# Performance work log

Hardware: AMD Instinct MI355X
Metric: run time of the kernel (lower is better)

## Reference

```python
import jax, jax.numpy as jnp
import numpy as np

T, B, N = 512, 256, 128


def setup_inputs() -> dict:
    key = jax.random.key(0)
    k1, k2, k3, k4, k5, k6 = jax.random.split(key, 6)
    emit = jax.random.normal(k1, (T, B, N), dtype=jnp.float32)
    target = jax.random.randint(k2, (T, B), 0, N)
    # prefix-true mask from random lengths in [1, T]
    lengths = jax.random.randint(k3, (B,), 1, T + 1)
    mask = jnp.arange(T)[:, None] < lengths[None, :]
    std = (1.0 / N) ** 0.5
    trans = jax.random.normal(k4, (N, N), dtype=jnp.float32) * std
    strans = jax.random.normal(k5, (N,), dtype=jnp.float32) * std
    etrans = jax.random.normal(k6, (N,), dtype=jnp.float32) * std
    return {"emit": emit, "target": target, "mask": mask,
            "trans": trans, "strans": strans, "etrans": etrans}


def _logZ(emit, mask, trans, strans, etrans):
    alpha0 = strans + emit[0]  # (B, N)

    def step(alpha, xs):
        e_t, m_t = xs  # (B, N), (B,)
        # scores[b, j] = logsumexp_i(alpha[b, i] + trans[i, j] + e_t[b, j])
        scores = jax.scipy.special.logsumexp(
            alpha[:, :, None] + trans[None, :, :] + e_t[:, None, :], axis=1)
        alpha = jnp.where(m_t[:, None], scores, alpha)
        return alpha, None

    alpha, _ = jax.lax.scan(step, alpha0, (emit[1:], mask[1:]))
    return jax.scipy.special.logsumexp(alpha + etrans, axis=1).sum()


def _score(emit, target, mask, trans, strans, etrans):
    Tn, Bn, _ = emit.shape
    # emission scores of gold tags: (T, B)
    sc = jnp.take_along_axis(emit, target[:, :, None], axis=2)[..., 0]
    # transition scores between consecutive gold tags
    sc = sc.at[1:].add(trans[target[:-1], target[1:]])
    score = jnp.sum(jnp.where(mask, sc, jnp.float32(0.0)))
    ends = mask.astype(jnp.int32).sum(axis=0) - 1  # (B,)
    score = score + strans[target[0]].sum()
    score = score + etrans[target[ends, jnp.arange(Bn)]].sum()
    return score


def reference(emit, target, mask, trans, strans, etrans):
    Bn = emit.shape[1]
    logZ = _logZ(emit, mask, trans, strans, etrans)
    score = _score(emit, target, mask, trans, strans, etrans)
    return (logZ - score) / Bn
```

## Files before the change

### kernel.cpp

```cpp
#include <hip/hip_runtime.h>

#define TT 512
#define BB 256
#define NN 128
#define MW 16
#define NWG (BB / MW)
#define STH 144

#define LENS_OFF 256
#define AF_OFF 2048
#define CF_OFF (AF_OFF + BB * NN * 4)
#define BU_OFF (CF_OFF + 1024)
#define CB_OFF (BU_OFF + BB * NN * 4)
#define XQ_OFF (CB_OFF + 1024)
#define XQ_SZ ((size_t)TT * BB * NN * 2)

typedef __attribute__((ext_vector_type(8))) short short8_t;
typedef __attribute__((ext_vector_type(4))) float f32x4;

__device__ __forceinline__ unsigned short f2bf(float f) {
  unsigned u = __float_as_uint(f);
  return (unsigned short)((u + 0x7FFF + ((u >> 16) & 1)) >> 16);
}
__device__ __forceinline__ float bf2f(unsigned short h) {
  return __uint_as_float(((unsigned)h) << 16);
}
__device__ __forceinline__ int orig_j(int p) {
  return 32 * (p >> 5) + 16 * (p & 1) + ((p >> 1) & 15);
}

__global__ __launch_bounds__(256) void crf_expemit(
    const float* __restrict__ emit, uint4* __restrict__ Xq) {
  const int bid = blockIdx.x;
  const int g = bid >> 9;
  const int t = bid & (TT - 1);
  const int tid = threadIdx.x;
  const int w = tid >> 6, l = tid & 63, qd = l >> 4, c = l & 15;
  const int bg = g * MW;
  unsigned pk[4];
#pragma unroll
  for (int r = 0; r < 4; ++r) {
    const size_t row = ((size_t)t * BB + bg + 4 * qd + r) * NN + 32 * w + c;
    float v0 = __expf(emit[row]);
    float v1 = __expf(emit[row + 16]);
    pk[r] = (unsigned)f2bf(v0) | ((unsigned)f2bf(v1) << 16);
  }
  Xq[((size_t)g * TT + t) * 256 + tid] = make_uint4(pk[0], pk[1], pk[2], pk[3]);
}

__global__ __launch_bounds__(BB) void crf_score_k(
    const float* __restrict__ emit, const int* __restrict__ target,
    const void* __restrict__ maskp, const float* __restrict__ trans,
    const float* __restrict__ strans, const float* __restrict__ etrans,
    float* __restrict__ ws, int* __restrict__ lens) {
  __shared__ float rf[4];
  const int b = threadIdx.x;
  const int t = blockIdx.x;
  const unsigned char* mk8 = (const unsigned char*)maskp;
  const int* mk32 = (const int*)maskp;
  const bool is_u8 = (mk8[1] != 0);

  int m = is_u8 ? (mk8[t * BB + b] != 0) : (mk32[t * BB + b] != 0);
  float v = 0.f;
  if (m) {
    int tg = target[t * BB + b];
    v = emit[((size_t)t * BB + b) * NN + tg];
    v += (t > 0) ? trans[target[(t - 1) * BB + b] * NN + tg] : strans[tg];
    int mn = (t + 1 < TT) ? (is_u8 ? (mk8[(t + 1) * BB + b] != 0)
                                   : (mk32[(t + 1) * BB + b] != 0))
                          : 0;
    if (!mn) {
      v += etrans[tg];
      lens[b] = t + 1;
    }
  }
#pragma unroll
  for (int off = 32; off; off >>= 1) v += __shfl_down(v, off, 64);
  if ((b & 63) == 0) rf[b >> 6] = v;
  __syncthreads();
  if (b == 0) atomicAdd(&ws[1], rf[0] + rf[1] + rf[2] + rf[3]);
}

__global__ __launch_bounds__(256, 1) void crf_fb(
    const float* __restrict__ emit, const float* __restrict__ trans,
    const float* __restrict__ strans, const float* __restrict__ etrans,
    const uint4* __restrict__ Xq, const int* __restrict__ lens,
    float* __restrict__ AF, int* __restrict__ CF,
    float* __restrict__ BU, int* __restrict__ CB) {
  __shared__ __align__(16) unsigned short sV[2][MW * STH];
  __shared__ __align__(16) int nrm[2][MW];
  __shared__ __align__(16) int sC[MW];
  __shared__ int slen[MW];
  __shared__ int smax_s;

  const int tid = threadIdx.x;
  const int w = tid >> 6;
  const int l = tid & 63;
  const int c = l & 15;
  const int qd = l >> 4;
  const bool bwd = (blockIdx.x >= NWG);
  const int g = bwd ? (int)blockIdx.x - NWG : (int)blockIdx.x;
  const int bg = g * MW;

  if (tid == 0) smax_s = 0;
  if (tid < MW) slen[tid] = lens[bg + tid];
  __syncthreads();
  if (tid < MW) atomicMax(&smax_s, slen[tid]);

  short8_t eB[4][2];
#pragma unroll
  for (int kt = 0; kt < 4; ++kt)
#pragma unroll
    for (int u = 0; u < 2; ++u)
#pragma unroll
      for (int jj = 0; jj < 8; ++jj) {
        int kp = kt * 32 + qd * 8 + jj;
        int a_ = orig_j(kp);
        int b_ = 32 * w + 16 * u + c;
        float tv = bwd ? trans[b_ * NN + a_] : trans[a_ * NN + b_];
        eB[kt][u][jj] = (short)f2bf(__expf(tv));
      }
  const float eet0 = __expf(etrans[32 * w + c]);
  const float eet1 = __expf(etrans[32 * w + 16 + c]);

  {
    const int m = tid & 15;
    const int pbase = (tid >> 4) * 8;
    if (!bwd) {
      const int b = bg + m;
#pragma unroll
      for (int pp = 0; pp < 8; ++pp) {
        int p = pbase + pp;
        int j = orig_j(p);
        float v = __expf(strans[j] + emit[(size_t)b * NN + j]);
        sV[0][m * STH + p] = f2bf(v);
        if (p == 0)
          nrm[0][m] = ((int)((__float_as_uint(v) >> 23) & 0xFF)) - 120;
      }
    } else {
#pragma unroll
      for (int pp = 0; pp < 8; ++pp) {
        int p = pbase + pp;
        sV[0][m * STH + p] = 0x3F80;
        sV[1][m * STH + p] = 0x3F80;
        if (p == 0) { nrm[0][m] = 0; nrm[1][m] = 0; }
      }
    }
  }
  __syncthreads();
  const int smax = smax_s;
  int lm1[4];
#pragma unroll
  for (int r = 0; r < 4; ++r) lm1[r] = slen[4 * qd + r] - 1;

  int cloc[4] = {0, 0, 0, 0};
  const bool nwriter = (w == 0 && c == 0);
  const uint4* Xg = Xq + (size_t)g * TT * 256 + tid;

#define FB_MFMA()                                                             \
    const short8_t A0 = *(const short8_t*)&sV[PIN][c * STH + 0 + qd * 8];     \
    const short8_t A1 = *(const short8_t*)&sV[PIN][c * STH + 32 + qd * 8];    \
    const short8_t A2 = *(const short8_t*)&sV[PIN][c * STH + 64 + qd * 8];    \
    const short8_t A3 = *(const short8_t*)&sV[PIN][c * STH + 96 + qd * 8];    \
    const int4 nr = *(const int4*)&nrm[PIN][4 * qd];                          \
    f32x4 p0 = {0.f, 0.f, 0.f, 0.f}, q0 = {0.f, 0.f, 0.f, 0.f};              \
    f32x4 p1 = {0.f, 0.f, 0.f, 0.f}, q1 = {0.f, 0.f, 0.f, 0.f};              \
    p0 = __builtin_amdgcn_mfma_f32_16x16x32_bf16(A0, eB[0][0], p0, 0, 0, 0); \
    p1 = __builtin_amdgcn_mfma_f32_16x16x32_bf16(A0, eB[0][1], p1, 0, 0, 0); \
    q0 = __builtin_amdgcn_mfma_f32_16x16x32_bf16(A2, eB[2][0], q0, 0, 0, 0); \
    q1 = __builtin_amdgcn_mfma_f32_16x16x32_bf16(A2, eB[2][1], q1, 0, 0, 0); \
    p0 = __builtin_amdgcn_mfma_f32_16x16x32_bf16(A1, eB[1][0], p0, 0, 0, 0); \
    p1 = __builtin_amdgcn_mfma_f32_16x16x32_bf16(A1, eB[1][1], p1, 0, 0, 0); \
    q0 = __builtin_amdgcn_mfma_f32_16x16x32_bf16(A3, eB[3][0], q0, 0, 0, 0); \
    q1 = __builtin_amdgcn_mfma_f32_16x16x32_bf16(A3, eB[3][1], q1, 0, 0, 0); \
    const f32x4 ac0 = p0 + q0;                                                \
    const f32x4 ac1 = p1 + q1;                                                \
    const int nA[4] = {nr.x, nr.y, nr.z, nr.w};

  if (!bwd) {
    const int LmaxF = (smax < 258) ? smax : 258;
    for (int tb = 1; tb < LmaxF; tb += 8) {
      uint4 xq[8];
#pragma unroll
      for (int k = 0; k < 8; ++k) {
        int t = tb + k;
        if (t > TT - 1) t = TT - 1;
        xq[k] = Xg[(size_t)t * 256];
      }
#pragma unroll
      for (int k = 0; k < 8; ++k) {
        const int T_ = tb + k;
        if (T_ >= LmaxF) break;
        const int POUT = T_ & 1, PIN = POUT ^ 1;
        FB_MFMA();
        const unsigned xd[4] = {xq[k].x, xq[k].y, xq[k].z, xq[k].w};
        int nnw[4];
#pragma unroll
        for (int r_ = 0; r_ < 4; ++r_) {
          float x0 = __uint_as_float(xd[r_] << 16);
          float x1 = __uint_as_float(xd[r_] & 0xffff0000u);
          float v0 = ldexpf(ac0[r_] * x0, -nA[r_]);
          float v1 = ldexpf(ac1[r_] * x1, -nA[r_]);
          if (T_ <= lm1[r_]) {
            unsigned pk = (unsigned)f2bf(v0) | ((unsigned)f2bf(v1) << 16);
            *(unsigned*)&sV[POUT][(4 * qd + r_) * STH + 32 * w + 2 * c] = pk;
            cloc[r_] += nA[r_];
          }
          nnw[r_] = ((int)((__float_as_uint(v0) >> 23) & 0xFF)) - 120;
        }
        if (nwriter)
          *(int4*)&nrm[POUT][4 * qd] = make_int4(nnw[0], nnw[1], nnw[2], nnw[3]);
        __syncthreads();
      }
    }
  } else if (smax >= 259) {
    for (int tb = smax - 1; tb >= 258; tb -= 8) {
      uint4 xq[8];
#pragma unroll
      for (int k = 0; k < 8; ++k) {
        int t = tb - k;
        if (t < 258) t = 258;
        xq[k] = Xg[(size_t)t * 256];
      }
#pragma unroll
      for (int k = 0; k < 8; ++k) {
        const int T_ = tb - k;
        if (T_ < 258) break;
        const int POUT = T_ & 1, PIN = POUT ^ 1;
        FB_MFMA();
        const unsigned xd[4] = {xq[k].x, xq[k].y, xq[k].z, xq[k].w};
        int nnw[4];
#pragma unroll
        for (int r_ = 0; r_ < 4; ++r_) {
          float x0 = __uint_as_float(xd[r_] << 16);
          float x1 = __uint_as_float(xd[r_] & 0xffff0000u);
          const bool isact = (T_ == lm1[r_]);
          float v0 = isact ? x0 * eet0 : ldexpf(ac0[r_] * x0, -nA[r_]);
          float v1 = isact ? x1 * eet1 : ldexpf(ac1[r_] * x1, -nA[r_]);
          if (T_ <= lm1[r_]) {
            unsigned pk = (unsigned)f2bf(v0) | ((unsigned)f2bf(v1) << 16);
            *(unsigned*)&sV[POUT][(4 * qd + r_) * STH + 32 * w + 2 * c] = pk;
            cloc[r_] = isact ? 0 : cloc[r_] + nA[r_];
          }
          nnw[r_] = ((int)((__float_as_uint(v0) >> 23) & 0xFF)) - 120;
        }
        if (nwriter)
          *(int4*)&nrm[POUT][4 * qd] = make_int4(nnw[0], nnw[1], nnw[2], nnw[3]);
        __syncthreads();
      }
    }
  }
#undef FB_MFMA

  if (nwriter)
    *(int4*)&sC[4 * qd] = make_int4(cloc[0], cloc[1], cloc[2], cloc[3]);
  __syncthreads();
  {
    const int m = tid >> 4, i16 = tid & 15;
    if (!bwd) {
      int nf = slen[m] - 1;
      if (nf > 257) nf = 257;
      const int pf = nf & 1;
#pragma unroll
      for (int pp = 0; pp < 8; ++pp) {
        int p = i16 * 8 + pp;
        AF[(size_t)(bg + m) * NN + p] = bf2f(sV[pf][m * STH + p]);
      }
      if (i16 == 0) CF[bg + m] = sC[m];
    } else {
#pragma unroll
      for (int pp = 0; pp < 8; ++pp) {
        int p = i16 * 8 + pp;
        BU[(size_t)(bg + m) * NN + p] = bf2f(sV[0][m * STH + p]);
      }
      if (i16 == 0) CB[bg + m] = sC[m];
    }
  }
}

__global__ __launch_bounds__(256) void crf_comb(
    const float* __restrict__ trans, const float* __restrict__ etrans,
    const int* __restrict__ lens, const float* __restrict__ AF,
    const int* __restrict__ CF, const float* __restrict__ BU,
    const int* __restrict__ CB, float* __restrict__ ws,
    float* __restrict__ out) {
  __shared__ __align__(16) unsigned short sU[MW * STH];
  __shared__ float sRed[4][MW][2];
  __shared__ int slen[MW];
  const int tid = threadIdx.x;
  const int w = tid >> 6, l = tid & 63, c = l & 15, qd = l >> 4;
  const int g = blockIdx.x, bg = g * MW;

  if (tid < MW) slen[tid] = lens[bg + tid];
  {
    const int m = tid & 15, pbase = (tid >> 4) * 8;
#pragma unroll
    for (int pp = 0; pp < 8; ++pp) {
      int p = pbase + pp;
      sU[m * STH + p] = f2bf(BU[(size_t)(bg + m) * NN + p]);
    }
  }
  short8_t eB[4][2];
#pragma unroll
  for (int kt = 0; kt < 4; ++kt)
#pragma unroll
    for (int u = 0; u < 2; ++u)
#pragma unroll
      for (int jj = 0; jj < 8; ++jj) {
        int kp = kt * 32 + qd * 8 + jj;
        int a_ = orig_j(kp);
        int b_ = 32 * w + 16 * u + c;
        eB[kt][u][jj] = (short)f2bf(__expf(trans[b_ * NN + a_]));
      }
  const float eet0 = __expf(etrans[32 * w + c]);
  const float eet1 = __expf(etrans[32 * w + 16 + c]);
  __syncthreads();

  const short8_t A0 = *(const short8_t*)&sU[c * STH + 0 + qd * 8];
  const short8_t A1 = *(const short8_t*)&sU[c * STH + 32 + qd * 8];
  const short8_t A2 = *(const short8_t*)&sU[c * STH + 64 + qd * 8];
  const short8_t A3 = *(const short8_t*)&sU[c * STH + 96 + qd * 8];
  f32x4 ac0 = {0.f, 0.f, 0.f, 0.f}, ac1 = {0.f, 0.f, 0.f, 0.f};
  ac0 = __builtin_amdgcn_mfma_f32_16x16x32_bf16(A0, eB[0][0], ac0, 0, 0, 0);
  ac1 = __builtin_amdgcn_mfma_f32_16x16x32_bf16(A0, eB[0][1], ac1, 0, 0, 0);
  ac0 = __builtin_amdgcn_mfma_f32_16x16x32_bf16(A1, eB[1][0], ac0, 0, 0, 0);
  ac1 = __builtin_amdgcn_mfma_f32_16x16x32_bf16(A1, eB[1][1], ac1, 0, 0, 0);
  ac0 = __builtin_amdgcn_mfma_f32_16x16x32_bf16(A2, eB[2][0], ac0, 0, 0, 0);
  ac1 = __builtin_amdgcn_mfma_f32_16x16x32_bf16(A2, eB[2][1], ac1, 0, 0, 0);
  ac0 = __builtin_amdgcn_mfma_f32_16x16x32_bf16(A3, eB[3][0], ac0, 0, 0, 0);
  ac1 = __builtin_amdgcn_mfma_f32_16x16x32_bf16(A3, eB[3][1], ac1, 0, 0, 0);

#pragma unroll
  for (int r_ = 0; r_ < 4; ++r_) {
    float a0 = AF[(size_t)(bg + 4 * qd + r_) * NN + 32 * w + 2 * c];
    float a1 = AF[(size_t)(bg + 4 * qd + r_) * NN + 32 * w + 2 * c + 1];
    float dB = a0 * ac0[r_] + a1 * ac1[r_];
    float dA = a0 * eet0 + a1 * eet1;
#pragma unroll
    for (int mk = 1; mk < 16; mk <<= 1) {
      dB += __shfl_xor(dB, mk, 64);
      dA += __shfl_xor(dA, mk, 64);
    }
    if (c == 0) {
      sRed[w][4 * qd + r_][0] = dB;
      sRed[w][4 * qd + r_][1] = dA;
    }
  }
  __syncthreads();
  if (tid < MW) {
    float DB = sRed[0][tid][0] + sRed[1][tid][0] + sRed[2][tid][0] + sRed[3][tid][0];
    float DA = sRed[0][tid][1] + sRed[1][tid][1] + sRed[2][tid][1] + sRed[3][tid][1];
    const int len = slen[tid];
    const float LN2 = 0.6931471805599453f;
    float logZ;
    if (len >= 259)
      logZ = LN2 * (float)(CF[bg + tid] + CB[bg + tid]) + __logf(DB);
    else
      logZ = LN2 * (float)CF[bg + tid] + __logf(DA);
    atomicAdd(&ws[0], logZ);
  }
  __syncthreads();
  if (tid == 0) {
    __threadfence();
    unsigned old = atomicAdd((unsigned*)ws + 3, 1u);
    if (old == NWG - 1) {
      float zz = atomicAdd(&ws[0], 0.f);
      float ss = atomicAdd(&ws[1], 0.f);
      out[0] = (zz - ss) * (1.0f / (float)BB);
    }
  }
}

__global__ __launch_bounds__(256, 1) void crf_fused_fb(
    const float* __restrict__ emit, const int* __restrict__ target,
    const void* __restrict__ maskp, const float* __restrict__ trans,
    const float* __restrict__ strans, const float* __restrict__ etrans,
    float* __restrict__ ws, float* __restrict__ out) {
  __shared__ __align__(16) unsigned short sV[2][MW * STH];
  __shared__ __align__(16) int nrm[2][MW];
  __shared__ __align__(16) int sC[MW];
  __shared__ int slen[MW];
  __shared__ float sscore;
  __shared__ int smax;

  const int tid = threadIdx.x;
  const int w = tid >> 6;
  const int l = tid & 63;
  const int c = l & 15;
  const int qd = l >> 4;
  const int bg = blockIdx.x * MW;

  if (tid < MW) slen[tid] = 0;
  if (tid == 0) { sscore = 0.f; smax = 0; }
  __syncthreads();

  const unsigned char* mk8 = (const unsigned char*)maskp;
  const int* mk32 = (const int*)maskp;
  const bool is_u8 = (mk8[1] != 0);
  {
    const int mi = tid & 15;
    const int b = bg + mi;
    const int t0 = (tid >> 4) * 32;
    int cnt = 0;
    float sc = 0.f;
    for (int s = 0; s < 32; ++s) {
      int t = t0 + s;
      int m = is_u8 ? (mk8[t * BB + b] != 0) : (mk32[t * BB + b] != 0);
      if (m) {
        cnt++;
        int tg = target[t * BB + b];
        float v = emit[((size_t)t * BB + b) * NN + tg];
        v += (t > 0) ? trans[target[(t - 1) * BB + b] * NN + tg] : strans[tg];
        int mn = (t + 1 < TT) ? (is_u8 ? (mk8[(t + 1) * BB + b] != 0)
                                       : (mk32[(t + 1) * BB + b] != 0))
                              : 0;
        if (!mn) v += etrans[tg];
        sc += v;
      }
    }
    atomicAdd(&slen[mi], cnt);
    atomicAdd(&sscore, sc);
  }

  short8_t eB[4][2];
#pragma unroll
  for (int kt = 0; kt < 4; ++kt)
#pragma unroll
    for (int u = 0; u < 2; ++u)
#pragma unroll
      for (int jj = 0; jj < 8; ++jj) {
        int kp = kt * 32 + qd * 8 + jj;
        int i = orig_j(kp);
        int j = 32 * w + 16 * u + c;
        eB[kt][u][jj] = (short)f2bf(__expf(trans[i * NN + j]));
      }

  {
    const int m = tid & 15;
    const int b = bg + m;
    const int pbase = (tid >> 4) * 8;
#pragma unroll
    for (int pp = 0; pp < 8; ++pp) {
      int p = pbase + pp;
      int j = orig_j(p);
      float v = __expf(strans[j] + emit[(size_t)b * NN + j]);
      sV[0][m * STH + p] = f2bf(v);
      if (p == 0)
        nrm[0][m] = ((int)((__float_as_uint(v) >> 23) & 0xFF)) - 120;
    }
  }
  __syncthreads();

  if (tid < MW) atomicMax(&smax, slen[tid]);
  if (tid == 0) atomicAdd(&ws[1], sscore);
  __syncthreads();
  const int Lmax = smax;
  int lenr[4];
#pragma unroll
  for (int r = 0; r < 4; ++r) lenr[r] = slen[4 * qd + r];

  int off8[8];
#pragma unroll
  for (int r = 0; r < 4; ++r)
#pragma unroll
    for (int u = 0; u < 2; ++u)
      off8[r * 2 + u] = (bg + 4 * qd + r) * NN + 32 * w + 16 * u + c;

  float ra[8], rb[8], xv[8];
  {
#pragma unroll
    for (int i = 0; i < 8; ++i) ra[i] = emit[(size_t)1 * BB * NN + off8[i]];
#pragma unroll
    for (int i = 0; i < 8; ++i) rb[i] = emit[(size_t)2 * BB * NN + off8[i]];
#pragma unroll
    for (int i = 0; i < 8; ++i) xv[i] = __expf(ra[i]);
  }
  int cloc[4] = {0, 0, 0, 0};
  const bool nwriter = (w == 0 && c == 0);

#define CRF_STEP(T_, PIN, POUT, RL, RO)                                       \
  do {                                                                        \
    int tl = ((T_) + 2 < TT) ? (T_) + 2 : TT - 1;                             \
    const size_t gbase = (size_t)tl * (BB * NN);                              \
    _Pragma("unroll") for (int i_ = 0; i_ < 8; ++i_)                          \
        RL[i_] = emit[gbase + off8[i_]];                                      \
    const short8_t A0 = *(const short8_t*)&sV[PIN][c * STH + 0 + qd * 8];     \
    const short8_t A1 = *(const short8_t*)&sV[PIN][c * STH + 32 + qd * 8];    \
    const short8_t A2 = *(const short8_t*)&sV[PIN][c * STH + 64 + qd * 8];    \
    const short8_t A3 = *(const short8_t*)&sV[PIN][c * STH + 96 + qd * 8];    \
    const int4 nr = *(const int4*)&nrm[PIN][4 * qd];                          \
    f32x4 ac0 = {0.f, 0.f, 0.f, 0.f}, ac1 = {0.f, 0.f, 0.f, 0.f};             \
    ac0 = __builtin_amdgcn_mfma_f32_16x16x32_bf16(A0, eB[0][0], ac0, 0, 0, 0);\
    ac1 = __builtin_amdgcn_mfma_f32_16x16x32_bf16(A0, eB[0][1], ac1, 0, 0, 0);\
    ac0 = __builtin_amdgcn_mfma_f32_16x16x32_bf16(A1, eB[1][0], ac0, 0, 0, 0);\
    ac1 = __builtin_amdgcn_mfma_f32_16x16x32_bf16(A1, eB[1][1], ac1, 0, 0, 0);\
    ac0 = __builtin_amdgcn_mfma_f32_16x16x32_bf16(A2, eB[2][0], ac0, 0, 0, 0);\
    ac1 = __builtin_amdgcn_mfma_f32_16x16x32_bf16(A2, eB[2][1], ac1, 0, 0, 0);\
    ac0 = __builtin_amdgcn_mfma_f32_16x16x32_bf16(A3, eB[3][0], ac0, 0, 0, 0);\
    ac1 = __builtin_amdgcn_mfma_f32_16x16x32_bf16(A3, eB[3][1], ac1, 0, 0, 0);\
    const int nA[4] = {nr.x, nr.y, nr.z, nr.w};                               \
    int nnw[4];                                                               \
    _Pragma("unroll") for (int r_ = 0; r_ < 4; ++r_) {                        \
      float y0 = ac0[r_] * xv[2 * r_];                                        \
      float y1 = ac1[r_] * xv[2 * r_ + 1];                                    \
      float v0 = ldexpf(y0, -nA[r_]);                                         \
      float v1 = ldexpf(y1, -nA[r_]);                                         \
      if ((T_) < lenr[r_]) {                                                  \
        unsigned pk = (unsigned)f2bf(v0) | ((unsigned)f2bf(v1) << 16);        \
        *(unsigned*)&sV[POUT][(4 * qd + r_) * STH + 32 * w + 2 * c] = pk;     \
        cloc[r_] += nA[r_];                                                   \
      }                                                                       \
      nnw[r_] = ((int)((__float_as_uint(v0) >> 23) & 0xFF)) - 120;            \
    }                                                                         \
    if (nwriter)                                                              \
      *(int4*)&nrm[POUT][4 * qd] = make_int4(nnw[0], nnw[1], nnw[2], nnw[3]); \
    _Pragma("unroll") for (int i_ = 0; i_ < 8; ++i_)                          \
        xv[i_] = __expf(RO[i_]);                                              \
    __syncthreads();                                                          \
  } while (0)

  for (int t = 1; t < Lmax; t += 2) {
    CRF_STEP(t, 0, 1, ra, rb);
    if (t + 1 < Lmax) {
      CRF_STEP(t + 1, 1, 0, rb, ra);
    }
  }
#undef CRF_STEP

  if (nwriter) *(int4*)&sC[4 * qd] = make_int4(cloc[0], cloc[1], cloc[2], cloc[3]);
  __syncthreads();
  {
    const int m = tid >> 4, i16 = tid & 15;
    const int pb = (slen[m] - 1) & 1;
    float s = 0.f;
#pragma unroll
    for (int pp = 0; pp < 8; ++pp) {
      int p = i16 * 8 + pp;
      int j = orig_j(p);
      s += bf2f(sV[pb][m * STH + p]) * __expf(etrans[j]);
    }
    s += __shfl_xor(s, 1, 64);
    s += __shfl_xor(s, 2, 64);
    s += __shfl_xor(s, 4, 64);
    s += __shfl_xor(s, 8, 64);
    if (i16 == 0)
      atomicAdd(&ws[0], (float)sC[m] * 0.69314718f + __logf(s));
  }
  __syncthreads();
  if (tid == 0) {
    __threadfence();
    unsigned old = atomicAdd((unsigned*)ws + 3, 1u);
    if (old == NWG - 1) {
      float zz = atomicAdd(&ws[0], 0.f);
      float ss = atomicAdd(&ws[1], 0.f);
      out[0] = (zz - ss) * (1.0f / (float)BB);
    }
  }
}

extern "C" void kernel_launch(void* const* d_in, const int* in_sizes, int n_in,
                              void* d_out, int out_size, void* d_ws, size_t ws_size,
                              hipStream_t stream) {
  const float* emit = (const float*)d_in[0];
  const int* target = (const int*)d_in[1];
  const void* mask = (const void*)d_in[2];
  const float* trans = (const float*)d_in[3];
  const float* strans = (const float*)d_in[4];
  const float* etrans = (const float*)d_in[5];
  float* ws = (float*)d_ws;
  float* out = (float*)d_out;

  const size_t need = (size_t)XQ_OFF + XQ_SZ;
  hipMemsetAsync(d_ws, 0, 16, stream);
  if (ws_size >= need) {
    int* lens = (int*)((char*)d_ws + LENS_OFF);
    float* AF = (float*)((char*)d_ws + AF_OFF);
    int* CF = (int*)((char*)d_ws + CF_OFF);
    float* BU = (float*)((char*)d_ws + BU_OFF);
    int* CB = (int*)((char*)d_ws + CB_OFF);
    uint4* Xq = (uint4*)((char*)d_ws + XQ_OFF);
    crf_expemit<<<NWG * TT, 256, 0, stream>>>(emit, Xq);
    crf_score_k<<<TT, BB, 0, stream>>>(emit, target, mask, trans, strans,
                                       etrans, ws, lens);
    crf_fb<<<2 * NWG, 256, 0, stream>>>(emit, trans, strans, etrans,
                                        (const uint4*)Xq, lens, AF, CF, BU, CB);
    crf_comb<<<NWG, 256, 0, stream>>>(trans, etrans, lens, AF, CF, BU, CB, ws,
                                      out);
  } else {
    crf_fused_fb<<<NWG, 256, 0, stream>>>(emit, target, mask, trans, strans,
                                          etrans, ws, out);
  }
}
```

Measured before the change: 260.0 us.

## Run CRF forward/backward recurrence in a single wave with register-resident state

Replaces the 256-thread forward/backward kernel, which exchanged state through LDS with a barrier every timestep, with a 64-thread single-wave kernel covering 32 sequences. State stays in registers, and the next step's operand is rebuilt with packed bf16 conversion plus permlane32 swaps. The matmul moves to 32x32x16 MFMA, and renormalisation now runs only every fourth step. The exp-emission pre-pass is relaid out to match the new fragment ordering, with vectorised loads. In exchange, half as many workgroups (16 instead of 32) run the serial recurrence, and skipping renormalisation on most steps risks overflow or underflow.

```diff
diff --git a/kernel.cpp b/kernel.cpp
--- a/kernel.cpp
+++ b/kernel.cpp
@@ -5,6 +5,7 @@
 #define NN 128
 #define MW 16
 #define NWG (BB / MW)
+#define G2 8
 #define STH 144
 
 #define LENS_OFF 256
@@ -17,6 +18,7 @@
 
 typedef __attribute__((ext_vector_type(8))) short short8_t;
 typedef __attribute__((ext_vector_type(4))) float f32x4;
+typedef __attribute__((ext_vector_type(16))) float f32x16;
 
 __device__ __forceinline__ unsigned short f2bf(float f) {
   unsigned u = __float_as_uint(f);
@@ -28,24 +30,36 @@
 __device__ __forceinline__ int orig_j(int p) {
   return 32 * (p >> 5) + 16 * (p & 1) + ((p >> 1) & 15);
 }
-
-__global__ __launch_bounds__(256) void crf_expemit(
+__device__ __forceinline__ int pos_p(int j) {
+  return 32 * (j >> 5) + 2 * (j & 15) + ((j >> 4) & 1);
+}
+
+#define U4GET(v_, i_) \
+  ((i_) == 0 ? (v_).x : (i_) == 1 ? (v_).y : (i_) == 2 ? (v_).z : (v_).w)
+
+__global__ __launch_bounds__(256) void crf_expemit2(
     const float* __restrict__ emit, uint4* __restrict__ Xq) {
-  const int bid = blockIdx.x;
-  const int g = bid >> 9;
-  const int t = bid & (TT - 1);
-  const int tid = threadIdx.x;
-  const int w = tid >> 6, l = tid & 63, qd = l >> 4, c = l & 15;
-  const int bg = g * MW;
-  unsigned pk[4];
-#pragma unroll
-  for (int r = 0; r < 4; ++r) {
-    const size_t row = ((size_t)t * BB + bg + 4 * qd + r) * NN + 32 * w + c;
-    float v0 = __expf(emit[row]);
-    float v1 = __expf(emit[row + 16]);
-    pk[r] = (unsigned)f2bf(v0) | ((unsigned)f2bf(v1) << 16);
-  }
-  Xq[((size_t)g * TT + t) * 256 + tid] = make_uint4(pk[0], pk[1], pk[2], pk[3]);
+  const int wid = blockIdx.x * 4 + (threadIdx.x >> 6);
+  const int l = threadIdx.x & 63;
+  const int c5 = l & 31, h = l >> 5;
+  const int g = wid >> 9;
+  const int t = wid & (TT - 1);
+  const int b = g * 32 + c5;
+  const float* row = emit + ((size_t)t * BB + b) * NN;
+  unsigned wd[32];
+#pragma unroll
+  for (int q = 0; q < 16; ++q) {
+    const float4 f = *(const float4*)(row + 8 * q + 4 * h);
+    const float a0 = __expf(f.x), a1 = __expf(f.y);
+    const float a2 = __expf(f.z), a3 = __expf(f.w);
+    wd[2 * q] = (unsigned)f2bf(a0) | ((unsigned)f2bf(a1) << 16);
+    wd[2 * q + 1] = (unsigned)f2bf(a2) | ((unsigned)f2bf(a3) << 16);
+  }
+  uint4* out = Xq + ((size_t)g * TT + t) * 512 + l;
+#pragma unroll
+  for (int whi = 0; whi < 8; ++whi)
+    out[whi * 64] =
+        make_uint4(wd[4 * whi], wd[4 * whi + 1], wd[4 * whi + 2], wd[4 * whi + 3]);
 }
 
 __global__ __launch_bounds__(BB) void crf_score_k(
@@ -81,199 +95,279 @@
   if (b == 0) atomicAdd(&ws[1], rf[0] + rf[1] + rf[2] + rf[3]);
 }
 
-__global__ __launch_bounds__(256, 1) void crf_fb(
+__device__ __forceinline__ void dump_state(const float (&v0a)[4][4][2],
+                                           const float (&v1a)[4][4][2],
+                                           float* __restrict__ OUT, int b,
+                                           int h) {
+#pragma unroll
+  for (int T = 0; T < 4; ++T)
+#pragma unroll
+    for (int m = 0; m < 4; ++m)
+#pragma unroll
+      for (int rp = 0; rp < 2; ++rp) {
+        const int j0 = 32 * T + 8 * m + 4 * h + 2 * rp;
+        OUT[b * NN + pos_p(j0)] = v0a[T][m][rp];
+        OUT[b * NN + pos_p(j0 + 1)] = v1a[T][m][rp];
+      }
+}
+
+__device__ __forceinline__ void cvtperm(const float (&v0a)[4][4][2],
+                                        const float (&v1a)[4][4][2],
+                                        uint4 (&Bq)[8]) {
+  unsigned W[4][4][2];
+#pragma unroll
+  for (int T = 0; T < 4; ++T)
+#pragma unroll
+    for (int m = 0; m < 4; ++m)
+#pragma unroll
+      for (int rp = 0; rp < 2; ++rp) {
+        unsigned wv;
+        asm("v_cvt_pk_bf16_f32 %0, %1, %2"
+            : "=v"(wv)
+            : "v"(v0a[T][m][rp]), "v"(v1a[T][m][rp]));
+        W[T][m][rp] = wv;
+      }
+#pragma unroll
+  for (int T = 0; T < 4; ++T)
+#pragma unroll
+    for (int a = 0; a < 2; ++a) {
+      unsigned X0 = W[T][2 * a][0], Y0 = W[T][2 * a + 1][0];
+      unsigned X1 = W[T][2 * a][1], Y1 = W[T][2 * a + 1][1];
+      asm("v_permlane32_swap_b32 %0, %1" : "+v"(X0), "+v"(Y0));
+      asm("v_permlane32_swap_b32 %0, %1" : "+v"(X1), "+v"(Y1));
+      Bq[2 * T + a] = make_uint4(X0, X1, Y0, Y1);
+    }
+}
+
+template <bool BWD>
+__device__ __forceinline__ void fb_step(
+    int t, bool donorm, bool dfinal, int tpre, int lm1, int c5, int h, int b,
+    const uint4* __restrict__ Xg, const short8_t (&eA)[4][8],
+    const f32x16& kZ, uint4 (&Bq)[8], uint4 (&xw)[8], int& cloc,
+    const float* __restrict__ etrans, float* __restrict__ OUT,
+    int* __restrict__ CNT) {
+  union U8 { uint4 u; short8_t s; };
+  f32x16 dd[4];
+  {
+    U8 bc;
+    bc.u = Bq[0];
+#pragma unroll
+    for (int T = 0; T < 4; ++T)
+      dd[T] = __builtin_amdgcn_mfma_f32_32x32x16_bf16(eA[T][0], bc.s, kZ, 0, 0, 0);
+  }
+#pragma unroll
+  for (int k = 1; k < 8; ++k) {
+    U8 bc;
+    bc.u = Bq[k];
+#pragma unroll
+    for (int T = 0; T < 4; ++T)
+      dd[T] =
+          __builtin_amdgcn_mfma_f32_32x32x16_bf16(eA[T][k], bc.s, dd[T], 0, 0, 0);
+  }
+  uint4 xv[8];
+#pragma unroll
+  for (int i = 0; i < 8; ++i) xv[i] = xw[i];
+  {
+    const uint4* src = Xg + (size_t)tpre * 512;
+#pragma unroll
+    for (int i = 0; i < 8; ++i) xw[i] = src[i * 64];
+  }
+  float v0a[4][4][2], v1a[4][4][2];
+#pragma unroll
+  for (int T = 0; T < 4; ++T)
+#pragma unroll
+    for (int m = 0; m < 4; ++m)
+#pragma unroll
+      for (int rp = 0; rp < 2; ++rp) {
+        const int w = 8 * T + 2 * m + rp;
+        const unsigned xu = U4GET(xv[w >> 2], w & 3);
+        const float xl = __uint_as_float(xu << 16);
+        const float xh = __uint_as_float(xu & 0xffff0000u);
+        v0a[T][m][rp] = dd[T][4 * m + 2 * rp] * xl;
+        v1a[T][m][rp] = dd[T][4 * m + 2 * rp + 1] * xh;
+      }
+  if (donorm) {
+    unsigned eb = __float_as_uint(v0a[0][0][0]);
+    unsigned ec = eb;
+    asm("v_permlane32_swap_b32 %0, %1" : "+v"(eb), "+v"(ec));
+    const int n = (int)((eb >> 23) & 0xFFu) - 127;
+    cloc += n;
+    const int nn = -n;
+#pragma unroll
+    for (int T = 0; T < 4; ++T)
+#pragma unroll
+      for (int m = 0; m < 4; ++m)
+#pragma unroll
+        for (int rp = 0; rp < 2; ++rp) {
+          v0a[T][m][rp] = ldexpf(v0a[T][m][rp], nn);
+          v1a[T][m][rp] = ldexpf(v1a[T][m][rp], nn);
+        }
+  }
+  if (BWD) {
+    const bool act = (t == lm1);
+    if (__any(act)) {
+#pragma unroll
+      for (int T = 0; T < 4; ++T)
+#pragma unroll
+        for (int m = 0; m < 4; ++m)
+#pragma unroll
+          for (int rp = 0; rp < 2; ++rp) {
+            const int j0 = 32 * T + 8 * m + 4 * h + 2 * rp;
+            const int w = 8 * T + 2 * m + rp;
+            const unsigned xu = U4GET(xv[w >> 2], w & 3);
+            const float xl = __uint_as_float(xu << 16);
+            const float xh = __uint_as_float(xu & 0xffff0000u);
+            const float a0 = xl * __expf(etrans[j0]);
+            const float a1 = xh * __expf(etrans[j0 + 1]);
+            v0a[T][m][rp] = act ? a0 : v0a[T][m][rp];
+            v1a[T][m][rp] = act ? a1 : v1a[T][m][rp];
+          }
+      cloc = act ? 0 : cloc;
+    }
+    if (dfinal) {
+      const bool dmp = (lm1 >= 258);
+      if (__any(dmp)) {
+        if (dmp) {
+          dump_state(v0a, v1a, OUT, b, h);
+          if (h == 0) CNT[b] = cloc;
+        }
+      }
+    }
+  } else {
+    const bool fz = (t == lm1) || (dfinal && lm1 > t);
+    if (__any(fz)) {
+      if (fz) {
+        dump_state(v0a, v1a, OUT, b, h);
+        if (h == 0) CNT[b] = cloc;
+      }
+    }
+  }
+  cvtperm(v0a, v1a, Bq);
+}
+
+__global__ __launch_bounds__(64, 1) void crf_fb2(
     const float* __restrict__ emit, const float* __restrict__ trans,
     const float* __restrict__ strans, const float* __restrict__ etrans,
     const uint4* __restrict__ Xq, const int* __restrict__ lens,
-    float* __restrict__ AF, int* __restrict__ CF,
-    float* __restrict__ BU, int* __restrict__ CB) {
-  __shared__ __align__(16) unsigned short sV[2][MW * STH];
-  __shared__ __align__(16) int nrm[2][MW];
-  __shared__ __align__(16) int sC[MW];
-  __shared__ int slen[MW];
-  __shared__ int smax_s;
-
-  const int tid = threadIdx.x;
-  const int w = tid >> 6;
-  const int l = tid & 63;
-  const int c = l & 15;
-  const int qd = l >> 4;
-  const bool bwd = (blockIdx.x >= NWG);
-  const int g = bwd ? (int)blockIdx.x - NWG : (int)blockIdx.x;
-  const int bg = g * MW;
-
-  if (tid == 0) smax_s = 0;
-  if (tid < MW) slen[tid] = lens[bg + tid];
-  __syncthreads();
-  if (tid < MW) atomicMax(&smax_s, slen[tid]);
-
-  short8_t eB[4][2];
-#pragma unroll
-  for (int kt = 0; kt < 4; ++kt)
-#pragma unroll
-    for (int u = 0; u < 2; ++u)
+    float* __restrict__ AF, int* __restrict__ CF, float* __restrict__ BU,
+    int* __restrict__ CB) {
+  const int l = threadIdx.x & 63;
+  const int c5 = l & 31, h = l >> 5;
+  const bool bwd = (blockIdx.x >= G2);
+  const int g = bwd ? (int)blockIdx.x - G2 : (int)blockIdx.x;
+  const int b = g * 32 + c5;
+
+  const int len = lens[b];
+  const int lm1 = len - 1;
+  int sm = len;
+#pragma unroll
+  for (int mk = 1; mk < 32; mk <<= 1) {
+    int o = __shfl_xor(sm, mk, 64);
+    sm = o > sm ? o : sm;
+  }
+
+  short8_t eA[4][8];
+#pragma unroll
+  for (int T = 0; T < 4; ++T)
+#pragma unroll
+    for (int kt = 0; kt < 8; ++kt) {
+      short8_t f;
 #pragma unroll
       for (int jj = 0; jj < 8; ++jj) {
-        int kp = kt * 32 + qd * 8 + jj;
-        int a_ = orig_j(kp);
-        int b_ = 32 * w + 16 * u + c;
-        float tv = bwd ? trans[b_ * NN + a_] : trans[a_ * NN + b_];
-        eB[kt][u][jj] = (short)f2bf(__expf(tv));
-      }
-  const float eet0 = __expf(etrans[32 * w + c]);
-  const float eet1 = __expf(etrans[32 * w + 16 + c]);
-
-  {
-    const int m = tid & 15;
-    const int pbase = (tid >> 4) * 8;
-    if (!bwd) {
-      const int b = bg + m;
-#pragma unroll
-      for (int pp = 0; pp < 8; ++pp) {
-        int p = pbase + pp;
-        int j = orig_j(p);
-        float v = __expf(strans[j] + emit[(size_t)b * NN + j]);
-        sV[0][m * STH + p] = f2bf(v);
-        if (p == 0)
-          nrm[0][m] = ((int)((__float_as_uint(v) >> 23) & 0xFF)) - 120;
-      }
-    } else {
-#pragma unroll
-      for (int pp = 0; pp < 8; ++pp) {
-        int p = pbase + pp;
-        sV[0][m * STH + p] = 0x3F80;
-        sV[1][m * STH + p] = 0x3F80;
-        if (p == 0) { nrm[0][m] = 0; nrm[1][m] = 0; }
-      }
-    }
-  }
-  __syncthreads();
-  const int smax = smax_s;
-  int lm1[4];
-#pragma unroll
-  for (int r = 0; r < 4; ++r) lm1[r] = slen[4 * qd + r] - 1;
-
-  int cloc[4] = {0, 0, 0, 0};
-  const bool nwriter = (w == 0 && c == 0);
-  const uint4* Xg = Xq + (size_t)g * TT * 256 + tid;
-
-#define FB_MFMA()                                                             \
-    const short8_t A0 = *(const short8_t*)&sV[PIN][c * STH + 0 + qd * 8];     \
-    const short8_t A1 = *(const short8_t*)&sV[PIN][c * STH + 32 + qd * 8];    \
-    const short8_t A2 = *(const short8_t*)&sV[PIN][c * STH + 64 + qd * 8];    \
-    const short8_t A3 = *(const short8_t*)&sV[PIN][c * STH + 96 + qd * 8];    \
-    const int4 nr = *(const int4*)&nrm[PIN][4 * qd];                          \
-    f32x4 p0 = {0.f, 0.f, 0.f, 0.f}, q0 = {0.f, 0.f, 0.f, 0.f};              \
-    f32x4 p1 = {0.f, 0.f, 0.f, 0.f}, q1 = {0.f, 0.f, 0.f, 0.f};              \
-    p0 = __builtin_amdgcn_mfma_f32_16x16x32_bf16(A0, eB[0][0], p0, 0, 0, 0); \
-    p1 = __builtin_amdgcn_mfma_f32_16x16x32_bf16(A0, eB[0][1], p1, 0, 0, 0); \
-    q0 = __builtin_amdgcn_mfma_f32_16x16x32_bf16(A2, eB[2][0], q0, 0, 0, 0); \
-    q1 = __builtin_amdgcn_mfma_f32_16x16x32_bf16(A2, eB[2][1], q1, 0, 0, 0); \
-    p0 = __builtin_amdgcn_mfma_f32_16x16x32_bf16(A1, eB[1][0], p0, 0, 0, 0); \
-    p1 = __builtin_amdgcn_mfma_f32_16x16x32_bf16(A1, eB[1][1], p1, 0, 0, 0); \
-    q0 = __builtin_amdgcn_mfma_f32_16x16x32_bf16(A3, eB[3][0], q0, 0, 0, 0); \
-    q1 = __builtin_amdgcn_mfma_f32_16x16x32_bf16(A3, eB[3][1], q1, 0, 0, 0); \
-    const f32x4 ac0 = p0 + q0;                                                \
-    const f32x4 ac1 = p1 + q1;                                                \
-    const int nA[4] = {nr.x, nr.y, nr.z, nr.w};
+        const int jm = 32 * T + c5;
+        const int kk = 16 * kt + 8 * h + jj;
+        const float tv = bwd ? trans[jm * NN + kk] : trans[kk * NN + jm];
+        f[jj] = (short)f2bf(__expf(tv));
+      }
+      eA[T][kt] = f;
+    }
+
+  f32x16 kZ;
+#pragma unroll
+  for (int i = 0; i < 16; ++i) kZ[i] = 0.f;
+
+  const uint4* Xg = Xq + (size_t)g * TT * 512 + l;
+  uint4 Bq[8];
+  int cloc = 0;
 
   if (!bwd) {
-    const int LmaxF = (smax < 258) ? smax : 258;
-    for (int tb = 1; tb < LmaxF; tb += 8) {
-      uint4 xq[8];
-#pragma unroll
-      for (int k = 0; k < 8; ++k) {
-        int t = tb + k;
-        if (t > TT - 1) t = TT - 1;
-        xq[k] = Xg[(size_t)t * 256];
-      }
-#pragma unroll
-      for (int k = 0; k < 8; ++k) {
-        const int T_ = tb + k;
-        if (T_ >= LmaxF) break;
-        const int POUT = T_ & 1, PIN = POUT ^ 1;
-        FB_MFMA();
-        const unsigned xd[4] = {xq[k].x, xq[k].y, xq[k].z, xq[k].w};
-        int nnw[4];
-#pragma unroll
-        for (int r_ = 0; r_ < 4; ++r_) {
-          float x0 = __uint_as_float(xd[r_] << 16);
-          float x1 = __uint_as_float(xd[r_] & 0xffff0000u);
-          float v0 = ldexpf(ac0[r_] * x0, -nA[r_]);
-          float v1 = ldexpf(ac1[r_] * x1, -nA[r_]);
-          if (T_ <= lm1[r_]) {
-            unsigned pk = (unsigned)f2bf(v0) | ((unsigned)f2bf(v1) << 16);
-            *(unsigned*)&sV[POUT][(4 * qd + r_) * STH + 32 * w + 2 * c] = pk;
-            cloc[r_] += nA[r_];
-          }
-          nnw[r_] = ((int)((__float_as_uint(v0) >> 23) & 0xFF)) - 120;
+    float v0a[4][4][2], v1a[4][4][2];
+#pragma unroll
+    for (int T = 0; T < 4; ++T)
+#pragma unroll
+      for (int m = 0; m < 4; ++m)
+#pragma unroll
+        for (int rp = 0; rp < 2; ++rp) {
+          const int j0 = 32 * T + 8 * m + 4 * h + 2 * rp;
+          v0a[T][m][rp] = __expf(strans[j0] + emit[(size_t)b * NN + j0]);
+          v1a[T][m][rp] = __expf(strans[j0 + 1] + emit[(size_t)b * NN + j0 + 1]);
         }
-        if (nwriter)
-          *(int4*)&nrm[POUT][4 * qd] = make_int4(nnw[0], nnw[1], nnw[2], nnw[3]);
-        __syncthreads();
-      }
-    }
-  } else if (smax >= 259) {
-    for (int tb = smax - 1; tb >= 258; tb -= 8) {
-      uint4 xq[8];
-#pragma unroll
-      for (int k = 0; k < 8; ++k) {
-        int t = tb - k;
-        if (t < 258) t = 258;
-        xq[k] = Xg[(size_t)t * 256];
-      }
-#pragma unroll
-      for (int k = 0; k < 8; ++k) {
-        const int T_ = tb - k;
-        if (T_ < 258) break;
-        const int POUT = T_ & 1, PIN = POUT ^ 1;
-        FB_MFMA();
-        const unsigned xd[4] = {xq[k].x, xq[k].y, xq[k].z, xq[k].w};
-        int nnw[4];
-#pragma unroll
-        for (int r_ = 0; r_ < 4; ++r_) {
-          float x0 = __uint_as_float(xd[r_] << 16);
-          float x1 = __uint_as_float(xd[r_] & 0xffff0000u);
-          const bool isact = (T_ == lm1[r_]);
-          float v0 = isact ? x0 * eet0 : ldexpf(ac0[r_] * x0, -nA[r_]);
-          float v1 = isact ? x1 * eet1 : ldexpf(ac1[r_] * x1, -nA[r_]);
-          if (T_ <= lm1[r_]) {
-            unsigned pk = (unsigned)f2bf(v0) | ((unsigned)f2bf(v1) << 16);
-            *(unsigned*)&sV[POUT][(4 * qd + r_) * STH + 32 * w + 2 * c] = pk;
-            cloc[r_] = isact ? 0 : cloc[r_] + nA[r_];
-          }
-          nnw[r_] = ((int)((__float_as_uint(v0) >> 23) & 0xFF)) - 120;
-        }
-        if (nwriter)
-          *(int4*)&nrm[POUT][4 * qd] = make_int4(nnw[0], nnw[1], nnw[2], nnw[3]);
-        __syncthreads();
-      }
-    }
-  }
-#undef FB_MFMA
-
-  if (nwriter)
-    *(int4*)&sC[4 * qd] = make_int4(cloc[0], cloc[1], cloc[2], cloc[3]);
-  __syncthreads();
-  {
-    const int m = tid >> 4, i16 = tid & 15;
-    if (!bwd) {
-      int nf = slen[m] - 1;
-      if (nf > 257) nf = 257;
-      const int pf = nf & 1;
-#pragma unroll
-      for (int pp = 0; pp < 8; ++pp) {
-        int p = i16 * 8 + pp;
-        AF[(size_t)(bg + m) * NN + p] = bf2f(sV[pf][m * STH + p]);
-      }
-      if (i16 == 0) CF[bg + m] = sC[m];
-    } else {
-#pragma unroll
-      for (int pp = 0; pp < 8; ++pp) {
-        int p = i16 * 8 + pp;
-        BU[(size_t)(bg + m) * NN + p] = bf2f(sV[0][m * STH + p]);
-      }
-      if (i16 == 0) CB[bg + m] = sC[m];
+    if (__any(lm1 == 0)) {
+      if (lm1 == 0) {
+        dump_state(v0a, v1a, AF, b, h);
+        if (h == 0) CF[b] = 0;
+      }
+    }
+    cvtperm(v0a, v1a, Bq);
+
+    const int Lmax = sm < 258 ? sm : 258;
+    const int S = Lmax - 1;
+    uint4 xbuf0[8], xbuf1[8];
+    {
+      const uint4* p0 = Xg + (size_t)1 * 512;
+      const uint4* p1 = Xg + (size_t)2 * 512;
+#pragma unroll
+      for (int i = 0; i < 8; ++i) xbuf0[i] = p0[i * 64];
+#pragma unroll
+      for (int i = 0; i < 8; ++i) xbuf1[i] = p1[i * 64];
+    }
+    int s = 0;
+#define STEPF(SS, NRM, XB)                                               \
+  fb_step<false>(1 + (SS), (NRM), ((SS) + 1 == S),                       \
+                 ((SS) + 3 < TT ? (SS) + 3 : TT - 1), lm1, c5, h, b, Xg, \
+                 eA, kZ, Bq, XB, cloc, etrans, AF, CF)
+    for (; s + 4 <= S; s += 4) {
+      STEPF(s + 0, false, xbuf0);
+      STEPF(s + 1, false, xbuf1);
+      STEPF(s + 2, false, xbuf0);
+      STEPF(s + 3, true, xbuf1);
+    }
+    if (s + 0 < S) STEPF(s + 0, false, xbuf0);
+    if (s + 1 < S) STEPF(s + 1, false, xbuf1);
+    if (s + 2 < S) STEPF(s + 2, false, xbuf0);
+#undef STEPF
+  } else {
+#pragma unroll
+    for (int k = 0; k < 8; ++k)
+      Bq[k] = make_uint4(0x3F803F80u, 0x3F803F80u, 0x3F803F80u, 0x3F803F80u);
+    if (sm >= 259) {
+      const int tstart = sm - 1;
+      const int S = tstart - 257;
+      uint4 xbuf0[8], xbuf1[8];
+      {
+        const uint4* p0 = Xg + (size_t)tstart * 512;
+        const int t1 = tstart - 1;
+        const uint4* p1 = Xg + (size_t)t1 * 512;
+#pragma unroll
+        for (int i = 0; i < 8; ++i) xbuf0[i] = p0[i * 64];
+#pragma unroll
+        for (int i = 0; i < 8; ++i) xbuf1[i] = p1[i * 64];
+      }
+      int s = 0;
+#define STEPB(SS, NRM, XB)                                                  \
+  fb_step<true>(tstart - (SS), (NRM), ((SS) + 1 == S),                      \
+                (tstart - (SS) - 2 > 0 ? tstart - (SS) - 2 : 0), lm1, c5,   \
+                h, b, Xg, eA, kZ, Bq, XB, cloc, etrans, BU, CB)
+      for (; s + 4 <= S; s += 4) {
+        STEPB(s + 0, false, xbuf0);
+        STEPB(s + 1, false, xbuf1);
+        STEPB(s + 2, false, xbuf0);
+        STEPB(s + 3, true, xbuf1);
+      }
+      if (s + 0 < S) STEPB(s + 0, false, xbuf0);
+      if (s + 1 < S) STEPB(s + 1, false, xbuf1);
+      if (s + 2 < S) STEPB(s + 2, false, xbuf0);
+#undef STEPB
     }
   }
 }
@@ -579,11 +673,11 @@
     float* BU = (float*)((char*)d_ws + BU_OFF);
     int* CB = (int*)((char*)d_ws + CB_OFF);
     uint4* Xq = (uint4*)((char*)d_ws + XQ_OFF);
-    crf_expemit<<<NWG * TT, 256, 0, stream>>>(emit, Xq);
+    crf_expemit2<<<G2 * TT / 4, 256, 0, stream>>>(emit, Xq);
     crf_score_k<<<TT, BB, 0, stream>>>(emit, target, mask, trans, strans,
                                        etrans, ws, lens);
-    crf_fb<<<2 * NWG, 256, 0, stream>>>(emit, trans, strans, etrans,
-                                        (const uint4*)Xq, lens, AF, CF, BU, CB);
+    crf_fb2<<<2 * G2, 64, 0, stream>>>(emit, trans, strans, etrans,
+                                       (const uint4*)Xq, lens, AF, CF, BU, CB);
     crf_comb<<<NWG, 256, 0, stream>>>(trans, etrans, lens, AF, CF, BU, CB, ws,
                                       out);
   } else {
```

Result: slower. 418.5 us (+61.0%).

## Merge forward and backward recursions into one 512-thread block per group

Applied to the files above, without the earlier changes.

Forward and backward CRF recursions for the same batch group were separate 256-thread blocks. They now run as two halves of one 512-thread block, with separate shared buffers per half and a common iteration loop and barrier. This halves the block count and places both directions on one CU, which may cut launch and scheduling overhead. The cost is that each half waits at barriers for the other half's timestep and loops to the longer of the two counts, and doubled register pressure could lower occupancy.

```diff
diff --git a/kernel.cpp b/kernel.cpp
--- a/kernel.cpp
+++ b/kernel.cpp
@@ -81,26 +81,31 @@
   if (b == 0) atomicAdd(&ws[1], rf[0] + rf[1] + rf[2] + rf[3]);
 }
 
-__global__ __launch_bounds__(256, 1) void crf_fb(
+__global__ __launch_bounds__(512, 1) void crf_fbf(
     const float* __restrict__ emit, const float* __restrict__ trans,
     const float* __restrict__ strans, const float* __restrict__ etrans,
     const uint4* __restrict__ Xq, const int* __restrict__ lens,
     float* __restrict__ AF, int* __restrict__ CF,
     float* __restrict__ BU, int* __restrict__ CB) {
-  __shared__ __align__(16) unsigned short sV[2][MW * STH];
-  __shared__ __align__(16) int nrm[2][MW];
-  __shared__ __align__(16) int sC[MW];
+  __shared__ __align__(16) unsigned short sV[2][2][MW * STH];
+  __shared__ __align__(16) int nrm[2][2][MW];
+  __shared__ __align__(16) int sC[2][MW];
   __shared__ int slen[MW];
   __shared__ int smax_s;
 
   const int tid = threadIdx.x;
-  const int w = tid >> 6;
-  const int l = tid & 63;
+  const int half = tid >> 8;
+  const int tid2 = tid & 255;
+  const int w = tid2 >> 6;
+  const int l = tid2 & 63;
   const int c = l & 15;
   const int qd = l >> 4;
-  const bool bwd = (blockIdx.x >= NWG);
-  const int g = bwd ? (int)blockIdx.x - NWG : (int)blockIdx.x;
+  const bool bwd = (half == 1);
+  const int g = blockIdx.x;
   const int bg = g * MW;
+
+  unsigned short(*sVh)[MW * STH] = sV[half];
+  int(*nrmh)[MW] = nrm[half];
 
   if (tid == 0) smax_s = 0;
   if (tid < MW) slen[tid] = lens[bg + tid];
@@ -124,8 +129,8 @@
   const float eet1 = __expf(etrans[32 * w + 16 + c]);
 
   {
-    const int m = tid & 15;
-    const int pbase = (tid >> 4) * 8;
+    const int m = tid2 & 15;
+    const int pbase = (tid2 >> 4) * 8;
     if (!bwd) {
       const int b = bg + m;
 #pragma unroll
@@ -133,17 +138,17 @@
         int p = pbase + pp;
         int j = orig_j(p);
         float v = __expf(strans[j] + emit[(size_t)b * NN + j]);
-        sV[0][m * STH + p] = f2bf(v);
+        sVh[0][m * STH + p] = f2bf(v);
         if (p == 0)
-          nrm[0][m] = ((int)((__float_as_uint(v) >> 23) & 0xFF)) - 120;
+          nrmh[0][m] = ((int)((__float_as_uint(v) >> 23) & 0xFF)) - 120;
       }
     } else {
 #pragma unroll
       for (int pp = 0; pp < 8; ++pp) {
         int p = pbase + pp;
-        sV[0][m * STH + p] = 0x3F80;
-        sV[1][m * STH + p] = 0x3F80;
-        if (p == 0) { nrm[0][m] = 0; nrm[1][m] = 0; }
+        sVh[0][m * STH + p] = 0x3F80;
+        sVh[1][m * STH + p] = 0x3F80;
+        if (p == 0) { nrmh[0][m] = 0; nrmh[1][m] = 0; }
       }
     }
   }
@@ -155,108 +160,95 @@
 
   int cloc[4] = {0, 0, 0, 0};
   const bool nwriter = (w == 0 && c == 0);
-  const uint4* Xg = Xq + (size_t)g * TT * 256 + tid;
-
-#define FB_MFMA()                                                             \
-    const short8_t A0 = *(const short8_t*)&sV[PIN][c * STH + 0 + qd * 8];     \
-    const short8_t A1 = *(const short8_t*)&sV[PIN][c * STH + 32 + qd * 8];    \
-    const short8_t A2 = *(const short8_t*)&sV[PIN][c * STH + 64 + qd * 8];    \
-    const short8_t A3 = *(const short8_t*)&sV[PIN][c * STH + 96 + qd * 8];    \
-    const int4 nr = *(const int4*)&nrm[PIN][4 * qd];                          \
-    f32x4 p0 = {0.f, 0.f, 0.f, 0.f}, q0 = {0.f, 0.f, 0.f, 0.f};              \
-    f32x4 p1 = {0.f, 0.f, 0.f, 0.f}, q1 = {0.f, 0.f, 0.f, 0.f};              \
-    p0 = __builtin_amdgcn_mfma_f32_16x16x32_bf16(A0, eB[0][0], p0, 0, 0, 0); \
-    p1 = __builtin_amdgcn_mfma_f32_16x16x32_bf16(A0, eB[0][1], p1, 0, 0, 0); \
-    q0 = __builtin_amdgcn_mfma_f32_16x16x32_bf16(A2, eB[2][0], q0, 0, 0, 0); \
-    q1 = __builtin_amdgcn_mfma_f32_16x16x32_bf16(A2, eB[2][1], q1, 0, 0, 0); \
-    p0 = __builtin_amdgcn_mfma_f32_16x16x32_bf16(A1, eB[1][0], p0, 0, 0, 0); \
-    p1 = __builtin_amdgcn_mfma_f32_16x16x32_bf16(A1, eB[1][1], p1, 0, 0, 0); \
-    q0 = __builtin_amdgcn_mfma_f32_16x16x32_bf16(A3, eB[3][0], q0, 0, 0, 0); \
-    q1 = __builtin_amdgcn_mfma_f32_16x16x32_bf16(A3, eB[3][1], q1, 0, 0, 0); \
-    const f32x4 ac0 = p0 + q0;                                                \
-    const f32x4 ac1 = p1 + q1;                                                \
-    const int nA[4] = {nr.x, nr.y, nr.z, nr.w};
-
-  if (!bwd) {
-    const int LmaxF = (smax < 258) ? smax : 258;
-    for (int tb = 1; tb < LmaxF; tb += 8) {
-      uint4 xq[8];
-#pragma unroll
-      for (int k = 0; k < 8; ++k) {
-        int t = tb + k;
+  const uint4* Xg = Xq + (size_t)g * TT * 256 + tid2;
+
+  const int LmaxF = (smax < 258) ? smax : 258;
+  const int NITf = LmaxF - 1;
+  const int NITb = (smax >= 259) ? smax - 258 : 0;
+  const int NIT = NITf > NITb ? NITf : NITb;
+  const int tstart = smax - 1;
+
+  for (int tb = 0; tb < NIT; tb += 8) {
+    uint4 xq[8];
+#pragma unroll
+    for (int k = 0; k < 8; ++k) {
+      int t;
+      if (!bwd) {
+        t = 1 + tb + k;
         if (t > TT - 1) t = TT - 1;
-        xq[k] = Xg[(size_t)t * 256];
-      }
-#pragma unroll
-      for (int k = 0; k < 8; ++k) {
-        const int T_ = tb + k;
-        if (T_ >= LmaxF) break;
+      } else {
+        t = tstart - (tb + k);
+        if (t < 0) t = 0;
+      }
+      xq[k] = Xg[(size_t)t * 256];
+    }
+#pragma unroll
+    for (int k = 0; k < 8; ++k) {
+      const int it = tb + k;
+      if (it >= NIT) break;
+      const bool active = bwd ? (it < NITb) : (it < NITf);
+      if (active) {
+        const int T_ = bwd ? (tstart - it) : (1 + it);
         const int POUT = T_ & 1, PIN = POUT ^ 1;
-        FB_MFMA();
+        const short8_t A0 = *(const short8_t*)&sVh[PIN][c * STH + 0 + qd * 8];
+        const short8_t A1 = *(const short8_t*)&sVh[PIN][c * STH + 32 + qd * 8];
+        const short8_t A2 = *(const short8_t*)&sVh[PIN][c * STH + 64 + qd * 8];
+        const short8_t A3 = *(const short8_t*)&sVh[PIN][c * STH + 96 + qd * 8];
+        const int4 nr = *(const int4*)&nrmh[PIN][4 * qd];
+        f32x4 p0 = {0.f, 0.f, 0.f, 0.f}, q0 = {0.f, 0.f, 0.f, 0.f};
+        f32x4 p1 = {0.f, 0.f, 0.f, 0.f}, q1 = {0.f, 0.f, 0.f, 0.f};
+        p0 = __builtin_amdgcn_mfma_f32_16x16x32_bf16(A0, eB[0][0], p0, 0, 0, 0);
+        p1 = __builtin_amdgcn_mfma_f32_16x16x32_bf16(A0, eB[0][1], p1, 0, 0, 0);
+        q0 = __builtin_amdgcn_mfma_f32_16x16x32_bf16(A2, eB[2][0], q0, 0, 0, 0);
+        q1 = __builtin_amdgcn_mfma_f32_16x16x32_bf16(A2, eB[2][1], q1, 0, 0, 0);
+        p0 = __builtin_amdgcn_mfma_f32_16x16x32_bf16(A1, eB[1][0], p0, 0, 0, 0);
+        p1 = __builtin_amdgcn_mfma_f32_16x16x32_bf16(A1, eB[1][1], p1, 0, 0, 0);
+        q0 = __builtin_amdgcn_mfma_f32_16x16x32_bf16(A3, eB[3][0], q0, 0, 0, 0);
+        q1 = __builtin_amdgcn_mfma_f32_16x16x32_bf16(A3, eB[3][1], q1, 0, 0, 0);
+        const f32x4 ac0 = p0 + q0;
+        const f32x4 ac1 = p1 + q1;
+        const int nA[4] = {nr.x, nr.y, nr.z, nr.w};
         const unsigned xd[4] = {xq[k].x, xq[k].y, xq[k].z, xq[k].w};
         int nnw[4];
 #pragma unroll
         for (int r_ = 0; r_ < 4; ++r_) {
           float x0 = __uint_as_float(xd[r_] << 16);
           float x1 = __uint_as_float(xd[r_] & 0xffff0000u);
-          float v0 = ldexpf(ac0[r_] * x0, -nA[r_]);
-          float v1 = ldexpf(ac1[r_] * x1, -nA[r_]);
-          if (T_ <= lm1[r_]) {
-            unsigned pk = (unsigned)f2bf(v0) | ((unsigned)f2bf(v1) << 16);
-            *(unsigned*)&sV[POUT][(4 * qd + r_) * STH + 32 * w + 2 * c] = pk;
-            cloc[r_] += nA[r_];
+          float v0, v1;
+          const bool wr = (T_ <= lm1[r_]);
+          if (!bwd) {
+            v0 = ldexpf(ac0[r_] * x0, -nA[r_]);
+            v1 = ldexpf(ac1[r_] * x1, -nA[r_]);
+            if (wr) {
+              unsigned pk = (unsigned)f2bf(v0) | ((unsigned)f2bf(v1) << 16);
+              *(unsigned*)&sVh[POUT][(4 * qd + r_) * STH + 32 * w + 2 * c] = pk;
+              cloc[r_] += nA[r_];
+            }
+          } else {
+            const bool isact = (T_ == lm1[r_]);
+            v0 = isact ? x0 * eet0 : ldexpf(ac0[r_] * x0, -nA[r_]);
+            v1 = isact ? x1 * eet1 : ldexpf(ac1[r_] * x1, -nA[r_]);
+            if (wr) {
+              unsigned pk = (unsigned)f2bf(v0) | ((unsigned)f2bf(v1) << 16);
+              *(unsigned*)&sVh[POUT][(4 * qd + r_) * STH + 32 * w + 2 * c] = pk;
+              cloc[r_] = isact ? 0 : cloc[r_] + nA[r_];
+            }
           }
           nnw[r_] = ((int)((__float_as_uint(v0) >> 23) & 0xFF)) - 120;
         }
         if (nwriter)
-          *(int4*)&nrm[POUT][4 * qd] = make_int4(nnw[0], nnw[1], nnw[2], nnw[3]);
-        __syncthreads();
-      }
-    }
-  } else if (smax >= 259) {
-    for (int tb = smax - 1; tb >= 258; tb -= 8) {
-      uint4 xq[8];
-#pragma unroll
-      for (int k = 0; k < 8; ++k) {
-        int t = tb - k;
-        if (t < 258) t = 258;
-        xq[k] = Xg[(size_t)t * 256];
-      }
-#pragma unroll
-      for (int k = 0; k < 8; ++k) {
-        const int T_ = tb - k;
-        if (T_ < 258) break;
-        const int POUT = T_ & 1, PIN = POUT ^ 1;
-        FB_MFMA();
-        const unsigned xd[4] = {xq[k].x, xq[k].y, xq[k].z, xq[k].w};
-        int nnw[4];
-#pragma unroll
-        for (int r_ = 0; r_ < 4; ++r_) {
-          float x0 = __uint_as_float(xd[r_] << 16);
-          float x1 = __uint_as_float(xd[r_] & 0xffff0000u);
-          const bool isact = (T_ == lm1[r_]);
-          float v0 = isact ? x0 * eet0 : ldexpf(ac0[r_] * x0, -nA[r_]);
-          float v1 = isact ? x1 * eet1 : ldexpf(ac1[r_] * x1, -nA[r_]);
-          if (T_ <= lm1[r_]) {
-            unsigned pk = (unsigned)f2bf(v0) | ((unsigned)f2bf(v1) << 16);
-            *(unsigned*)&sV[POUT][(4 * qd + r_) * STH + 32 * w + 2 * c] = pk;
-            cloc[r_] = isact ? 0 : cloc[r_] + nA[r_];
-          }
-          nnw[r_] = ((int)((__float_as_uint(v0) >> 23) & 0xFF)) - 120;
-        }
-        if (nwriter)
-          *(int4*)&nrm[POUT][4 * qd] = make_int4(nnw[0], nnw[1], nnw[2], nnw[3]);
-        __syncthreads();
-      }
-    }
-  }
-#undef FB_MFMA
+          *(int4*)&nrmh[POUT][4 * qd] =
+              make_int4(nnw[0], nnw[1], nnw[2], nnw[3]);
+      }
+      __syncthreads();
+    }
+  }
 
   if (nwriter)
-    *(int4*)&sC[4 * qd] = make_int4(cloc[0], cloc[1], cloc[2], cloc[3]);
-  __syncthreads();
-  {
-    const int m = tid >> 4, i16 = tid & 15;
+    *(int4*)&sC[half][4 * qd] = make_int4(cloc[0], cloc[1], cloc[2], cloc[3]);
+  __syncthreads();
+  {
+    const int m = tid2 >> 4, i16 = tid2 & 15;
     if (!bwd) {
       int nf = slen[m] - 1;
       if (nf > 257) nf = 257;
@@ -264,16 +256,16 @@
 #pragma unroll
       for (int pp = 0; pp < 8; ++pp) {
         int p = i16 * 8 + pp;
-        AF[(size_t)(bg + m) * NN + p] = bf2f(sV[pf][m * STH + p]);
-      }
-      if (i16 == 0) CF[bg + m] = sC[m];
+        AF[(size_t)(bg + m) * NN + p] = bf2f(sVh[pf][m * STH + p]);
+      }
+      if (i16 == 0) CF[bg + m] = sC[0][m];
     } else {
 #pragma unroll
       for (int pp = 0; pp < 8; ++pp) {
         int p = i16 * 8 + pp;
-        BU[(size_t)(bg + m) * NN + p] = bf2f(sV[0][m * STH + p]);
-      }
-      if (i16 == 0) CB[bg + m] = sC[m];
+        BU[(size_t)(bg + m) * NN + p] = bf2f(sVh[0][m * STH + p]);
+      }
+      if (i16 == 0) CB[bg + m] = sC[1][m];
     }
   }
 }
@@ -582,8 +574,8 @@
     crf_expemit<<<NWG * TT, 256, 0, stream>>>(emit, Xq);
     crf_score_k<<<TT, BB, 0, stream>>>(emit, target, mask, trans, strans,
                                        etrans, ws, lens);
-    crf_fb<<<2 * NWG, 256, 0, stream>>>(emit, trans, strans, etrans,
-                                        (const uint4*)Xq, lens, AF, CF, BU, CB);
+    crf_fbf<<<NWG, 512, 0, stream>>>(emit, trans, strans, etrans,
+                                     (const uint4*)Xq, lens, AF, CF, BU, CB);
     crf_comb<<<NWG, 256, 0, stream>>>(trans, etrans, lens, AF, CF, BU, CB, ws,
                                       out);
   } else {
```

Result: slower. 318.0 us (+22.3%).
